# Performance work log

Hardware: AMD Instinct MI355X
Metric: run time of the kernel (lower is better)

Reference implementation:

```python
import jax, jax.numpy as jnp
import numpy as np

B, S, E = 4, 2048, 1024
H, D = 16, 64
SCALE = D ** -0.5


def setup_inputs() -> dict:
    key = jax.random.key(0)
    ks = jax.random.split(key, 6)
    x = jax.random.normal(ks[0], (B, S, E), dtype=jnp.float32)
    # per-head projection weights stacked along head axis: [H, E, D]
    Wq = jax.random.normal(ks[1], (H, E, D), dtype=jnp.float32) * 0.02
    Wk = jax.random.normal(ks[2], (H, E, D), dtype=jnp.float32) * 0.02
    Wv = jax.random.normal(ks[3], (H, E, D), dtype=jnp.float32) * 0.02
    # output projection: concat(H*D) -> E, with bias (nn.Linear default)
    Wo = jax.random.normal(ks[4], (H * D, E), dtype=jnp.float32) * 0.02
    bo = jax.random.normal(ks[5], (E,), dtype=jnp.float32) * 0.02
    return {"x": x, "Wq": Wq, "Wk": Wk, "Wv": Wv, "Wo": Wo, "bo": bo}


def reference(x, Wq, Wk, Wv, Wo, bo):
    # batched QKV projections for all heads at once
    q = jnp.einsum('bse,hed->bhsd', x, Wq)
    k = jnp.einsum('bse,hed->bhsd', x, Wk)
    v = jnp.einsum('bse,hed->bhsd', x, Wv)
    # full (non-causal) attention, scores [b,h,s,s]
    scores = jnp.einsum('bhsd,bhtd->bhst', q, k) * SCALE
    attn = jax.nn.softmax(scores, axis=-1)
    o = jnp.einsum('bhst,bhtd->bhsd', attn, v)
    # concat heads in head order along feature dim -> [b,s,H*D]
    o = o.transpose(0, 2, 1, 3).reshape(x.shape[0], x.shape[1], -1)
    return o @ Wo + bo
```

## Files before the change

### kernel.cpp

```cpp
#include <hip/hip_runtime.h>
#include <hip/hip_fp16.h>
#include <stdint.h>

#define BB 4
#define SS 2048
#define EE 1024
#define HH 16
#define DD 64

typedef _Float16 half8 __attribute__((ext_vector_type(8)));
typedef __fp16 fp16x2 __attribute__((ext_vector_type(2)));
typedef float f32x2 __attribute__((ext_vector_type(2)));
typedef float f32x4 __attribute__((ext_vector_type(4)));
typedef float f32x16 __attribute__((ext_vector_type(16)));
typedef uint32_t u32;
typedef uint32_t u32x2 __attribute__((ext_vector_type(2)));

#define MFMA32(a, b, c) __builtin_amdgcn_mfma_f32_16x16x32_f16((a), (b), (c), 0, 0, 0)
#define MFMA3216(a, b, c) __builtin_amdgcn_mfma_f32_32x32x16_f16((a), (b), (c), 0, 0, 0)

#define GLD_LDS16(g, l)                                                        \
  __builtin_amdgcn_global_load_lds(                                            \
      (const __attribute__((address_space(1))) u32*)(const void*)(g),          \
      (__attribute__((address_space(3))) u32*)(void*)(l), 16, 0, 0)

static __device__ __forceinline__ u32 pkh(float a, float b) {
  union { fp16x2 h; u32 u; } z;
  z.h = __builtin_amdgcn_cvt_pkrtz(a, b);
  return z.u;
}

static __device__ __forceinline__ void plswap(u32& a, u32& b) {
  asm("v_permlane32_swap_b32 %0, %1" : "+v"(a), "+v"(b));
}

__global__ __launch_bounds__(256) void conv_x_k(const float* __restrict__ x,
                                                _Float16* __restrict__ xh) {
  size_t i = ((size_t)blockIdx.x * 256 + threadIdx.x) * 8;
  f32x4 a = *(const f32x4*)(x + i);
  f32x4 b = *(const f32x4*)(x + i + 4);
  half8 o;
  o[0] = (_Float16)a[0]; o[1] = (_Float16)a[1];
  o[2] = (_Float16)a[2]; o[3] = (_Float16)a[3];
  o[4] = (_Float16)b[0]; o[5] = (_Float16)b[1];
  o[6] = (_Float16)b[2]; o[7] = (_Float16)b[3];
  *(half8*)(xh + i) = o;
}

__global__ __launch_bounds__(256) void conv_w_k(const float* __restrict__ Wq,
                                                const float* __restrict__ Wk,
                                                const float* __restrict__ Wv,
                                                _Float16* __restrict__ Wt) {
  __shared__ float T[64][65];
  int bid = blockIdx.x;
  int sel = bid >> 8, rem = bid & 255;
  int h = rem >> 4, e0 = (rem & 15) * 64;
  const float* W = (sel == 0 ? Wq : sel == 1 ? Wk : Wv) + (size_t)h * EE * DD;
  float scale = (sel == 0) ? 0.18033688011112042f : 1.0f;
  int tid = threadIdx.x;
  {
    int e = tid >> 2, d0 = (tid & 3) * 16;
#pragma unroll
    for (int i = 0; i < 4; ++i) {
      f32x4 v = *(const f32x4*)(W + (size_t)(e0 + e) * DD + d0 + i * 4);
      T[e][d0 + i * 4 + 0] = v[0];
      T[e][d0 + i * 4 + 1] = v[1];
      T[e][d0 + i * 4 + 2] = v[2];
      T[e][d0 + i * 4 + 3] = v[3];
    }
  }
  __syncthreads();
  {
    int d = tid >> 2, c0 = (tid & 3) * 16;
    half8 o0, o1;
#pragma unroll
    for (int i = 0; i < 8; ++i) o0[i] = (_Float16)(T[c0 + i][d] * scale);
#pragma unroll
    for (int i = 0; i < 8; ++i) o1[i] = (_Float16)(T[c0 + 8 + i][d] * scale);
    _Float16* dst = Wt + ((size_t)sel * 1024 + h * 64 + d) * EE + e0 + c0;
    *(half8*)dst = o0;
    *(half8*)(dst + 8) = o1;
  }
}

__global__ __launch_bounds__(256) void conv_wo_k(const float* __restrict__ Wo,
                                                 _Float16* __restrict__ Wot) {
  __shared__ float T[64][65];
  int bid = blockIdx.x;
  int k0 = (bid >> 4) * 64, n0 = (bid & 15) * 64;
  int tid = threadIdx.x;
  {
    int k = tid >> 2, c0 = (tid & 3) * 16;
#pragma unroll
    for (int i = 0; i < 4; ++i) {
      f32x4 v = *(const f32x4*)(Wo + (size_t)(k0 + k) * EE + n0 + c0 + i * 4);
      T[k][c0 + i * 4 + 0] = v[0];
      T[k][c0 + i * 4 + 1] = v[1];
      T[k][c0 + i * 4 + 2] = v[2];
      T[k][c0 + i * 4 + 3] = v[3];
    }
  }
  __syncthreads();
  {
    int n = tid >> 2, c0 = (tid & 3) * 16;
    half8 o0, o1;
#pragma unroll
    for (int i = 0; i < 8; ++i) o0[i] = (_Float16)T[c0 + i][n];
#pragma unroll
    for (int i = 0; i < 8; ++i) o1[i] = (_Float16)T[c0 + 8 + i][n];
    _Float16* dst = Wot + (size_t)(n0 + n) * EE + k0 + c0;
    *(half8*)dst = o0;
    *(half8*)(dst + 8) = o1;
  }
}

__global__ __launch_bounds__(256) void vtrans_k(const _Float16* __restrict__ v,
                                                _Float16* __restrict__ vT) {
  __shared__ _Float16 T[64][72];
  int bid = blockIdx.x;
  int bh = bid >> 5, st = bid & 31;
  const _Float16* vp = v + (size_t)bh * SS * DD + (size_t)st * 64 * DD;
  _Float16* op = vT + (size_t)bh * DD * SS + (size_t)st * 64;
  int tid = threadIdx.x;
  {
    int r = tid >> 2, c0 = (tid & 3) * 16;
    half8 a = *(const half8*)(vp + (size_t)r * DD + c0);
    half8 b = *(const half8*)(vp + (size_t)r * DD + c0 + 8);
#pragma unroll
    for (int j = 0; j < 8; ++j) T[c0 + j][r] = a[j];
#pragma unroll
    for (int j = 0; j < 8; ++j) T[c0 + 8 + j][r] = b[j];
  }
  __syncthreads();
  {
    int d = tid >> 2, sc = (tid & 3) * 16;
    half8 o0 = *(const half8*)&T[d][sc];
    half8 o1 = *(const half8*)&T[d][sc + 8];
    *(half8*)(op + (size_t)d * SS + sc) = o0;
    *(half8*)(op + (size_t)d * SS + sc + 8) = o1;
  }
}

__global__ __launch_bounds__(256, 3) void qkv_proj_k(
    const _Float16* __restrict__ xh, const _Float16* __restrict__ Wt,
    _Float16* __restrict__ qkv) {
  __shared__ __align__(16) _Float16 As[128 * 32];
  __shared__ __align__(16) _Float16 Bs[128 * 32];
  int bid0 = blockIdx.x;
  int bid = (bid0 & 7) * 192 + (bid0 >> 3);
  int nblk = bid % 24, mblk = bid / 24;
  int row0 = mblk * 128, n0 = nblk * 128;
  int tid = threadIdx.x, lane = tid & 63, w = tid >> 6;
  int wm = w >> 1, wn = w & 1;
  int l15 = lane & 15, lhi = lane >> 4;

  f32x4 acc[4][4];
#pragma unroll
  for (int i = 0; i < 4; ++i)
#pragma unroll
    for (int j = 0; j < 4; ++j) acc[i][j] = (f32x4){0.f, 0.f, 0.f, 0.f};

  const char* Ab = (const char*)xh + (size_t)row0 * 2048;
  const char* Bb = (const char*)Wt + (size_t)n0 * 2048;
  int ob0 = w * 1024 + lane * 16;

  for (int k0 = 0; k0 < EE; k0 += 32) {
    __syncthreads();
    GLD_LDS16(Ab + (size_t)(ob0 >> 6) * 2048 + k0 * 2 + (ob0 & 63),
              (char*)As + w * 1024);
    GLD_LDS16(Ab + (size_t)((ob0 + 4096) >> 6) * 2048 + k0 * 2 + (ob0 & 63),
              (char*)As + 4096 + w * 1024);
    GLD_LDS16(Bb + (size_t)(ob0 >> 6) * 2048 + k0 * 2 + (ob0 & 63),
              (char*)Bs + w * 1024);
    GLD_LDS16(Bb + (size_t)((ob0 + 4096) >> 6) * 2048 + k0 * 2 + (ob0 & 63),
              (char*)Bs + 4096 + w * 1024);
    __syncthreads();
    half8 a[4], b[4];
#pragma unroll
    for (int mf = 0; mf < 4; ++mf)
      a[mf] = *(const half8*)(As + (wm * 64 + mf * 16 + l15) * 32 + 8 * lhi);
#pragma unroll
    for (int nf = 0; nf < 4; ++nf)
      b[nf] = *(const half8*)(Bs + (wn * 64 + nf * 16 + l15) * 32 + 8 * lhi);
#pragma unroll
    for (int mf = 0; mf < 4; ++mf)
#pragma unroll
      for (int nf = 0; nf < 4; ++nf)
        acc[mf][nf] = MFMA32(a[mf], b[nf], acc[mf][nf]);
  }

  const size_t KOFF = (size_t)BB * HH * SS * DD;
#pragma unroll
  for (int mf = 0; mf < 4; ++mf)
#pragma unroll
    for (int nf = 0; nf < 4; ++nf)
#pragma unroll
      for (int r = 0; r < 4; ++r) {
        int row = row0 + wm * 64 + mf * 16 + 4 * lhi + r;
        int n = n0 + wn * 64 + nf * 16 + l15;
        int sel = n >> 10, hh = (n >> 6) & 15, d = n & 63;
        int b_ = row >> 11, s = row & 2047;
        qkv[(size_t)sel * KOFF + (((size_t)b_ * HH + hh) * SS + s) * DD + d] =
            (_Float16)acc[mf][nf][r];
      }
}

__global__ __launch_bounds__(512, 1) void attn_k(
    const _Float16* __restrict__ qkv, const _Float16* __restrict__ vT,
    _Float16* __restrict__ ob) {
  __shared__ __align__(16) _Float16 Ks[2][64 * 64];
  __shared__ __align__(16) _Float16 Vs[2][64 * 64];

  const int bid0 = blockIdx.x;
  const int bid = (bid0 & 7) * 32 + (bid0 >> 3);
  const int bh = bid >> 2, qb = bid & 3;
  const int b_ = bh >> 4, h = bh & 15;
  const size_t KOFF = (size_t)BB * HH * SS * DD;
  const _Float16* qp = qkv + (size_t)bh * SS * DD;
  const char* kp = (const char*)(qkv + KOFF + (size_t)bh * SS * DD);
  const char* vtp = (const char*)(vT + (size_t)bh * DD * SS);

  const int tid = threadIdx.x, lane = tid & 63, w = tid >> 6;
  const int l31 = lane & 31, u = lane >> 5;
  const int q0 = qb * 512 + w * 64;

  half8 qf[4][2];
#pragma unroll
  for (int ekf = 0; ekf < 4; ++ekf)
#pragma unroll
    for (int nq = 0; nq < 2; ++nq)
      qf[ekf][nq] = *(const half8*)(qp +
          (size_t)(q0 + nq * 32 + l31) * DD + ekf * 16 + u * 8);

  f32x16 oa00 = {}, oa10 = {}, oa01 = {}, oa11 = {};
  f32x2 rs2_0 = {0.f, 0.f}, rs2_1 = {0.f, 0.f};

  const int trow = tid >> 3;
  const int scol = ((tid & 7) * 16) ^ (16 * (trow & 7));
  const int lds0 = tid * 16;
  const int xsw = 16 * (l31 & 7);
  const int NT = SS / 64;

  GLD_LDS16(kp + trow * 128 + scol, (char*)Ks[0] + lds0);
  GLD_LDS16(vtp + (size_t)trow * 4096 + scol, (char*)Vs[0] + lds0);
  __syncthreads();

  for (int it = 0; it < NT; ++it) {
    const int cur = it & 1;
    if (it + 1 < NT) {
      GLD_LDS16(kp + (size_t)(it + 1) * 8192 + trow * 128 + scol,
                (char*)Ks[cur ^ 1] + lds0);
      GLD_LDS16(vtp + (size_t)(it + 1) * 128 + (size_t)trow * 4096 + scol,
                (char*)Vs[cur ^ 1] + lds0);
    }
    const char* kb = (const char*)Ks[cur];
    const char* vb = (const char*)Vs[cur];

#pragma unroll
    for (int nt = 0; nt < 2; ++nt) {
      const char* krow = kb + (size_t)(32 * nt + l31) * 128;
      half8 kA0 = *(const half8*)(krow + ((16 * u) ^ xsw));
      half8 kA1 = *(const half8*)(krow + ((32 + 16 * u) ^ xsw));
      half8 kA2 = *(const half8*)(krow + ((64 + 16 * u) ^ xsw));
      half8 kA3 = *(const half8*)(krow + ((96 + 16 * u) ^ xsw));
      f32x16 s0 = {}, s1 = {};
      __builtin_amdgcn_s_setprio(1);
      s0 = MFMA3216(kA0, qf[0][0], s0);
      s1 = MFMA3216(kA0, qf[0][1], s1);
      s0 = MFMA3216(kA1, qf[1][0], s0);
      s1 = MFMA3216(kA1, qf[1][1], s1);
      s0 = MFMA3216(kA2, qf[2][0], s0);
      s1 = MFMA3216(kA2, qf[2][1], s1);
      s0 = MFMA3216(kA3, qf[3][0], s0);
      s1 = MFMA3216(kA3, qf[3][1], s1);
      __builtin_amdgcn_s_setprio(0);

      u32 w0[8], w1[8];
#pragma unroll
      for (int m = 0; m < 8; ++m) {
        float a0 = __builtin_amdgcn_exp2f(s0[2 * m]);
        float a1 = __builtin_amdgcn_exp2f(s0[2 * m + 1]);
        w0[m] = pkh(a0, a1);
        rs2_0 += (f32x2){a0, a1};
        float c0 = __builtin_amdgcn_exp2f(s1[2 * m]);
        float c1 = __builtin_amdgcn_exp2f(s1[2 * m + 1]);
        w1[m] = pkh(c0, c1);
        rs2_1 += (f32x2){c0, c1};
      }

#pragma unroll
      for (int kfl = 0; kfl < 2; ++kfl) {
        u32 p00 = w0[4 * kfl + 0], p02 = w0[4 * kfl + 2];
        u32 p01 = w0[4 * kfl + 1], p03 = w0[4 * kfl + 3];
        plswap(p00, p02);
        plswap(p01, p03);
        u32 p10 = w1[4 * kfl + 0], p12 = w1[4 * kfl + 2];
        u32 p11 = w1[4 * kfl + 1], p13 = w1[4 * kfl + 3];
        plswap(p10, p12);
        plswap(p11, p13);
        union { u32 q[4]; half8 h; } pb0, pb1;
        pb0.q[0] = p00; pb0.q[1] = p01; pb0.q[2] = p02; pb0.q[3] = p03;
        pb1.q[0] = p10; pb1.q[1] = p11; pb1.q[2] = p12; pb1.q[3] = p13;
        const int kf = 2 * nt + kfl;
        const char* vcol = vb + ((32 * kf + 16 * u) ^ xsw);
        half8 vA0 = *(const half8*)(vcol + (size_t)l31 * 128);
        half8 vA1 = *(const half8*)(vcol + (size_t)(32 + l31) * 128);
        __builtin_amdgcn_s_setprio(1);
        oa00 = MFMA3216(vA0, pb0.h, oa00);
        oa10 = MFMA3216(vA1, pb0.h, oa10);
        oa01 = MFMA3216(vA0, pb1.h, oa01);
        oa11 = MFMA3216(vA1, pb1.h, oa11);
        __builtin_amdgcn_s_setprio(0);
      }
    }
    __syncthreads();
  }

  float rs0 = rs2_0.x + rs2_0.y;
  float rs1 = rs2_1.x + rs2_1.y;
  float inv0 = 1.0f / (rs0 + __shfl_xor(rs0, 32, 64));
  float inv1 = 1.0f / (rs1 + __shfl_xor(rs1, 32, 64));

#define STORE_OA(OA, MD, NQ, INV)                                              \
  {                                                                            \
    _Float16* dst = ob + (size_t)(b_ * SS + q0 + 32 * (NQ) + l31) * 1024 +     \
                    h * 64 + 32 * (MD) + 4 * u;                                \
    _Pragma("unroll")                                                          \
    for (int rr = 0; rr < 4; ++rr) {                                           \
      u32x2 pr;                                                                \
      pr.x = pkh(OA[4 * rr + 0] * (INV), OA[4 * rr + 1] * (INV));              \
      pr.y = pkh(OA[4 * rr + 2] * (INV), OA[4 * rr + 3] * (INV));              \
      *(u32x2*)(dst + 8 * rr) = pr;                                            \
    }                                                                          \
  }
  STORE_OA(oa00, 0, 0, inv0)
  STORE_OA(oa10, 1, 0, inv0)
  STORE_OA(oa01, 0, 1, inv1)
  STORE_OA(oa11, 1, 1, inv1)
#undef STORE_OA
}

__global__ __launch_bounds__(256, 3) void oproj_k(
    const _Float16* __restrict__ ob, const _Float16* __restrict__ Wot,
    const float* __restrict__ bo, float* __restrict__ out) {
  __shared__ __align__(16) _Float16 As[128 * 32];
  __shared__ __align__(16) _Float16 Bs[128 * 32];
  int bid0 = blockIdx.x;
  int bid = (bid0 & 7) * 64 + (bid0 >> 3);
  int nblk = bid & 7, mblk = bid >> 3;
  int row0 = mblk * 128, n0 = nblk * 128;
  int tid = threadIdx.x, lane = tid & 63, w = tid >> 6;
  int wm = w >> 1, wn = w & 1;
  int l15 = lane & 15, lhi = lane >> 4;

  f32x4 acc[4][4];
#pragma unroll
  for (int i = 0; i < 4; ++i)
#pragma unroll
    for (int j = 0; j < 4; ++j) acc[i][j] = (f32x4){0.f, 0.f, 0.f, 0.f};

  const char* Ab = (const char*)ob + (size_t)row0 * 2048;
  const char* Bb = (const char*)Wot + (size_t)n0 * 2048;
  int ob0 = w * 1024 + lane * 16;

  for (int k0 = 0; k0 < EE; k0 += 32) {
    __syncthreads();
    GLD_LDS16(Ab + (size_t)(ob0 >> 6) * 2048 + k0 * 2 + (ob0 & 63),
              (char*)As + w * 1024);
    GLD_LDS16(Ab + (size_t)((ob0 + 4096) >> 6) * 2048 + k0 * 2 + (ob0 & 63),
              (char*)As + 4096 + w * 1024);
    GLD_LDS16(Bb + (size_t)(ob0 >> 6) * 2048 + k0 * 2 + (ob0 & 63),
              (char*)Bs + w * 1024);
    GLD_LDS16(Bb + (size_t)((ob0 + 4096) >> 6) * 2048 + k0 * 2 + (ob0 & 63),
              (char*)Bs + 4096 + w * 1024);
    __syncthreads();
    half8 a[4], b[4];
#pragma unroll
    for (int mf = 0; mf < 4; ++mf)
      a[mf] = *(const half8*)(As + (wm * 64 + mf * 16 + l15) * 32 + 8 * lhi);
#pragma unroll
    for (int nf = 0; nf < 4; ++nf)
      b[nf] = *(const half8*)(Bs + (wn * 64 + nf * 16 + l15) * 32 + 8 * lhi);
#pragma unroll
    for (int mf = 0; mf < 4; ++mf)
#pragma unroll
      for (int nf = 0; nf < 4; ++nf)
        acc[mf][nf] = MFMA32(a[mf], b[nf], acc[mf][nf]);
  }

#pragma unroll
  for (int mf = 0; mf < 4; ++mf)
#pragma unroll
    for (int nf = 0; nf < 4; ++nf) {
      int n = n0 + wn * 64 + nf * 16 + l15;
      float bias = bo[n];
#pragma unroll
      for (int r = 0; r < 4; ++r) {
        int row = row0 + wm * 64 + mf * 16 + 4 * lhi + r;
        out[(size_t)row * EE + n] = acc[mf][nf][r] + bias;
      }
    }
}

extern "C" void kernel_launch(void* const* d_in, const int* in_sizes, int n_in,
                              void* d_out, int out_size, void* d_ws, size_t ws_size,
                              hipStream_t stream) {
  const float* x  = (const float*)d_in[0];
  const float* Wq = (const float*)d_in[1];
  const float* Wk = (const float*)d_in[2];
  const float* Wv = (const float*)d_in[3];
  const float* Wo = (const float*)d_in[4];
  const float* bo = (const float*)d_in[5];
  float* out = (float*)d_out;

  const size_t KOFF = (size_t)BB * HH * SS * DD;
  _Float16* qkv = (_Float16*)d_ws;
  _Float16* obuf = qkv + 3 * KOFF;
  _Float16* xh = (_Float16*)d_out;
  _Float16* Wt = xh + (size_t)BB * SS * EE;
  _Float16* vTbuf = xh;
  _Float16* Wot = qkv;

  conv_x_k<<<dim3(4096), dim3(256), 0, stream>>>(x, xh);
  conv_w_k<<<dim3(768), dim3(256), 0, stream>>>(Wq, Wk, Wv, Wt);
  qkv_proj_k<<<dim3(64 * 24), dim3(256), 0, stream>>>(xh, Wt, qkv);
  vtrans_k<<<dim3(64 * 32), dim3(256), 0, stream>>>(qkv + 2 * KOFF, vTbuf);
  attn_k<<<dim3(256), dim3(512), 0, stream>>>(qkv, vTbuf, obuf);
  conv_wo_k<<<dim3(256), dim3(256), 0, stream>>>(Wo, Wot);
  oproj_k<<<dim3(64 * 8), dim3(256), 0, stream>>>(obuf, Wot, bo, out);
}
```

Baseline: 196.9 us.

## Fuse V transpose into QKV GEMM epilogue, double-buffer GEMMs, reshape attention blocks

The V output of the QKV projection is now transposed through LDS inside the GEMM epilogue and written directly in [b,h,d,s] layout, so the separate vtrans kernel and its extra global round-trip go away. Both GEMMs (QKV and output projection) get double-buffered LDS staging so the next K-slice loads while the current one is multiplied. The attention kernel moves from 512-thread single-block CUs to 256-thread blocks with two per CU, and a grid of 512. It also drops the s_setprio hints. The added LDS for the transpose tile and double buffers may reduce occupancy of the GEMM kernels.

```diff
diff --git a/kernel.cpp b/kernel.cpp
--- a/kernel.cpp
+++ b/kernel.cpp
@@ -114,38 +114,12 @@
   }
 }
 
-__global__ __launch_bounds__(256) void vtrans_k(const _Float16* __restrict__ v,
-                                                _Float16* __restrict__ vT) {
-  __shared__ _Float16 T[64][72];
-  int bid = blockIdx.x;
-  int bh = bid >> 5, st = bid & 31;
-  const _Float16* vp = v + (size_t)bh * SS * DD + (size_t)st * 64 * DD;
-  _Float16* op = vT + (size_t)bh * DD * SS + (size_t)st * 64;
-  int tid = threadIdx.x;
-  {
-    int r = tid >> 2, c0 = (tid & 3) * 16;
-    half8 a = *(const half8*)(vp + (size_t)r * DD + c0);
-    half8 b = *(const half8*)(vp + (size_t)r * DD + c0 + 8);
-#pragma unroll
-    for (int j = 0; j < 8; ++j) T[c0 + j][r] = a[j];
-#pragma unroll
-    for (int j = 0; j < 8; ++j) T[c0 + 8 + j][r] = b[j];
-  }
-  __syncthreads();
-  {
-    int d = tid >> 2, sc = (tid & 3) * 16;
-    half8 o0 = *(const half8*)&T[d][sc];
-    half8 o1 = *(const half8*)&T[d][sc + 8];
-    *(half8*)(op + (size_t)d * SS + sc) = o0;
-    *(half8*)(op + (size_t)d * SS + sc + 8) = o1;
-  }
-}
-
 __global__ __launch_bounds__(256, 3) void qkv_proj_k(
     const _Float16* __restrict__ xh, const _Float16* __restrict__ Wt,
     _Float16* __restrict__ qkv) {
-  __shared__ __align__(16) _Float16 As[128 * 32];
-  __shared__ __align__(16) _Float16 Bs[128 * 32];
+  __shared__ __align__(16) _Float16 As[2][128 * 32];
+  __shared__ __align__(16) _Float16 Bs[2][128 * 32];
+  __shared__ __align__(16) _Float16 Tt[64][136];
   int bid0 = blockIdx.x;
   int bid = (bid0 & 7) * 192 + (bid0 >> 3);
   int nblk = bid % 24, mblk = bid / 24;
@@ -164,65 +138,101 @@
   const char* Bb = (const char*)Wt + (size_t)n0 * 2048;
   int ob0 = w * 1024 + lane * 16;
 
+#define STAGE_AB(K0, BUF)                                                      \
+  {                                                                            \
+    GLD_LDS16(Ab + (size_t)(ob0 >> 6) * 2048 + (K0) * 2 + (ob0 & 63),          \
+              (char*)As[BUF] + w * 1024);                                      \
+    GLD_LDS16(Ab + (size_t)((ob0 + 4096) >> 6) * 2048 + (K0) * 2 + (ob0 & 63), \
+              (char*)As[BUF] + 4096 + w * 1024);                               \
+    GLD_LDS16(Bb + (size_t)(ob0 >> 6) * 2048 + (K0) * 2 + (ob0 & 63),          \
+              (char*)Bs[BUF] + w * 1024);                                      \
+    GLD_LDS16(Bb + (size_t)((ob0 + 4096) >> 6) * 2048 + (K0) * 2 + (ob0 & 63), \
+              (char*)Bs[BUF] + 4096 + w * 1024);                               \
+  }
+
+  STAGE_AB(0, 0);
+  __syncthreads();
+
   for (int k0 = 0; k0 < EE; k0 += 32) {
-    __syncthreads();
-    GLD_LDS16(Ab + (size_t)(ob0 >> 6) * 2048 + k0 * 2 + (ob0 & 63),
-              (char*)As + w * 1024);
-    GLD_LDS16(Ab + (size_t)((ob0 + 4096) >> 6) * 2048 + k0 * 2 + (ob0 & 63),
-              (char*)As + 4096 + w * 1024);
-    GLD_LDS16(Bb + (size_t)(ob0 >> 6) * 2048 + k0 * 2 + (ob0 & 63),
-              (char*)Bs + w * 1024);
-    GLD_LDS16(Bb + (size_t)((ob0 + 4096) >> 6) * 2048 + k0 * 2 + (ob0 & 63),
-              (char*)Bs + 4096 + w * 1024);
-    __syncthreads();
+    int cur = (k0 >> 5) & 1;
+    if (k0 + 32 < EE) STAGE_AB(k0 + 32, cur ^ 1);
     half8 a[4], b[4];
 #pragma unroll
     for (int mf = 0; mf < 4; ++mf)
-      a[mf] = *(const half8*)(As + (wm * 64 + mf * 16 + l15) * 32 + 8 * lhi);
+      a[mf] = *(const half8*)(As[cur] + (wm * 64 + mf * 16 + l15) * 32 + 8 * lhi);
 #pragma unroll
     for (int nf = 0; nf < 4; ++nf)
-      b[nf] = *(const half8*)(Bs + (wn * 64 + nf * 16 + l15) * 32 + 8 * lhi);
+      b[nf] = *(const half8*)(Bs[cur] + (wn * 64 + nf * 16 + l15) * 32 + 8 * lhi);
 #pragma unroll
     for (int mf = 0; mf < 4; ++mf)
 #pragma unroll
       for (int nf = 0; nf < 4; ++nf)
         acc[mf][nf] = MFMA32(a[mf], b[nf], acc[mf][nf]);
-  }
+    __syncthreads();
+  }
+#undef STAGE_AB
 
   const size_t KOFF = (size_t)BB * HH * SS * DD;
-#pragma unroll
-  for (int mf = 0; mf < 4; ++mf)
-#pragma unroll
-    for (int nf = 0; nf < 4; ++nf)
-#pragma unroll
-      for (int r = 0; r < 4; ++r) {
-        int row = row0 + wm * 64 + mf * 16 + 4 * lhi + r;
-        int n = n0 + wn * 64 + nf * 16 + l15;
-        int sel = n >> 10, hh = (n >> 6) & 15, d = n & 63;
-        int b_ = row >> 11, s = row & 2047;
-        qkv[(size_t)sel * KOFF + (((size_t)b_ * HH + hh) * SS + s) * DD + d] =
-            (_Float16)acc[mf][nf][r];
+  if (nblk < 16) {
+#pragma unroll
+    for (int mf = 0; mf < 4; ++mf)
+#pragma unroll
+      for (int nf = 0; nf < 4; ++nf)
+#pragma unroll
+        for (int r = 0; r < 4; ++r) {
+          int row = row0 + wm * 64 + mf * 16 + 4 * lhi + r;
+          int n = n0 + wn * 64 + nf * 16 + l15;
+          int sel = n >> 10, hh = (n >> 6) & 15, d = n & 63;
+          int b_ = row >> 11, s = row & 2047;
+          qkv[(size_t)sel * KOFF + (((size_t)b_ * HH + hh) * SS + s) * DD + d] =
+              (_Float16)acc[mf][nf][r];
+        }
+  } else {
+    int b_ = row0 >> 11, sbase = row0 & 2047;
+    _Float16* vout = qkv + 2 * KOFF;
+#pragma unroll
+    for (int half = 0; half < 2; ++half) {
+      if (half) __syncthreads();
+      if (wn == half) {
+#pragma unroll
+        for (int mf = 0; mf < 4; ++mf)
+#pragma unroll
+          for (int nf = 0; nf < 4; ++nf) {
+            union { _Float16 h[4]; u32x2 v; } t4;
+#pragma unroll
+            for (int r = 0; r < 4; ++r) t4.h[r] = (_Float16)acc[mf][nf][r];
+            *(u32x2*)&Tt[nf * 16 + l15][wm * 64 + mf * 16 + 4 * lhi] = t4.v;
+          }
       }
-}
-
-__global__ __launch_bounds__(512, 1) void attn_k(
-    const _Float16* __restrict__ qkv, const _Float16* __restrict__ vT,
-    _Float16* __restrict__ ob) {
+      __syncthreads();
+      int d = tid >> 2, c0 = (tid & 3) * 32;
+      int head = ((n0 >> 6) + half) & 15;
+      _Float16* dst =
+          vout + ((size_t)((b_ * 16 + head) * 64 + d)) * SS + sbase + c0;
+#pragma unroll
+      for (int j = 0; j < 4; ++j)
+        *(half8*)(dst + 8 * j) = *(const half8*)&Tt[d][c0 + 8 * j];
+    }
+  }
+}
+
+__global__ __launch_bounds__(256, 2) void attn_k(
+    const _Float16* __restrict__ qkv, _Float16* __restrict__ ob) {
   __shared__ __align__(16) _Float16 Ks[2][64 * 64];
   __shared__ __align__(16) _Float16 Vs[2][64 * 64];
 
   const int bid0 = blockIdx.x;
-  const int bid = (bid0 & 7) * 32 + (bid0 >> 3);
-  const int bh = bid >> 2, qb = bid & 3;
+  const int bid = (bid0 & 7) * 64 + (bid0 >> 3);
+  const int bh = bid >> 3, qb = bid & 7;
   const int b_ = bh >> 4, h = bh & 15;
   const size_t KOFF = (size_t)BB * HH * SS * DD;
   const _Float16* qp = qkv + (size_t)bh * SS * DD;
   const char* kp = (const char*)(qkv + KOFF + (size_t)bh * SS * DD);
-  const char* vtp = (const char*)(vT + (size_t)bh * DD * SS);
+  const char* vtp = (const char*)(qkv + 2 * KOFF + (size_t)bh * DD * SS);
 
   const int tid = threadIdx.x, lane = tid & 63, w = tid >> 6;
   const int l31 = lane & 31, u = lane >> 5;
-  const int q0 = qb * 512 + w * 64;
+  const int q0 = qb * 256 + w * 64;
 
   half8 qf[4][2];
 #pragma unroll
@@ -241,18 +251,23 @@
   const int xsw = 16 * (l31 & 7);
   const int NT = SS / 64;
 
-  GLD_LDS16(kp + trow * 128 + scol, (char*)Ks[0] + lds0);
-  GLD_LDS16(vtp + (size_t)trow * 4096 + scol, (char*)Vs[0] + lds0);
+#define STAGE_KV(IT, BUF)                                                      \
+  {                                                                            \
+    const char* sk_ = kp + (size_t)(IT) * 8192;                                \
+    const char* sv_ = vtp + (size_t)(IT) * 128;                                \
+    GLD_LDS16(sk_ + trow * 128 + scol, (char*)Ks[BUF] + lds0);                 \
+    GLD_LDS16(sk_ + (trow + 32) * 128 + scol, (char*)Ks[BUF] + 4096 + lds0);   \
+    GLD_LDS16(sv_ + (size_t)trow * 4096 + scol, (char*)Vs[BUF] + lds0);        \
+    GLD_LDS16(sv_ + (size_t)(trow + 32) * 4096 + scol,                         \
+              (char*)Vs[BUF] + 4096 + lds0);                                   \
+  }
+
+  STAGE_KV(0, 0);
   __syncthreads();
 
   for (int it = 0; it < NT; ++it) {
     const int cur = it & 1;
-    if (it + 1 < NT) {
-      GLD_LDS16(kp + (size_t)(it + 1) * 8192 + trow * 128 + scol,
-                (char*)Ks[cur ^ 1] + lds0);
-      GLD_LDS16(vtp + (size_t)(it + 1) * 128 + (size_t)trow * 4096 + scol,
-                (char*)Vs[cur ^ 1] + lds0);
-    }
+    if (it + 1 < NT) STAGE_KV(it + 1, cur ^ 1);
     const char* kb = (const char*)Ks[cur];
     const char* vb = (const char*)Vs[cur];
 
@@ -264,7 +279,6 @@
       half8 kA2 = *(const half8*)(krow + ((64 + 16 * u) ^ xsw));
       half8 kA3 = *(const half8*)(krow + ((96 + 16 * u) ^ xsw));
       f32x16 s0 = {}, s1 = {};
-      __builtin_amdgcn_s_setprio(1);
       s0 = MFMA3216(kA0, qf[0][0], s0);
       s1 = MFMA3216(kA0, qf[0][1], s1);
       s0 = MFMA3216(kA1, qf[1][0], s0);
@@ -273,7 +287,6 @@
       s1 = MFMA3216(kA2, qf[2][1], s1);
       s0 = MFMA3216(kA3, qf[3][0], s0);
       s1 = MFMA3216(kA3, qf[3][1], s1);
-      __builtin_amdgcn_s_setprio(0);
 
       u32 w0[8], w1[8];
 #pragma unroll
@@ -305,16 +318,15 @@
         const char* vcol = vb + ((32 * kf + 16 * u) ^ xsw);
         half8 vA0 = *(const half8*)(vcol + (size_t)l31 * 128);
         half8 vA1 = *(const half8*)(vcol + (size_t)(32 + l31) * 128);
-        __builtin_amdgcn_s_setprio(1);
         oa00 = MFMA3216(vA0, pb0.h, oa00);
         oa10 = MFMA3216(vA1, pb0.h, oa10);
         oa01 = MFMA3216(vA0, pb1.h, oa01);
         oa11 = MFMA3216(vA1, pb1.h, oa11);
-        __builtin_amdgcn_s_setprio(0);
       }
     }
     __syncthreads();
   }
+#undef STAGE_KV
 
   float rs0 = rs2_0.x + rs2_0.y;
   float rs1 = rs2_1.x + rs2_1.y;
@@ -343,8 +355,8 @@
 __global__ __launch_bounds__(256, 3) void oproj_k(
     const _Float16* __restrict__ ob, const _Float16* __restrict__ Wot,
     const float* __restrict__ bo, float* __restrict__ out) {
-  __shared__ __align__(16) _Float16 As[128 * 32];
-  __shared__ __align__(16) _Float16 Bs[128 * 32];
+  __shared__ __align__(16) _Float16 As[2][128 * 32];
+  __shared__ __align__(16) _Float16 Bs[2][128 * 32];
   int bid0 = blockIdx.x;
   int bid = (bid0 & 7) * 64 + (bid0 >> 3);
   int nblk = bid & 7, mblk = bid >> 3;
@@ -363,30 +375,39 @@
   const char* Bb = (const char*)Wot + (size_t)n0 * 2048;
   int ob0 = w * 1024 + lane * 16;
 
+#define STAGE_AB(K0, BUF)                                                      \
+  {                                                                            \
+    GLD_LDS16(Ab + (size_t)(ob0 >> 6) * 2048 + (K0) * 2 + (ob0 & 63),          \
+              (char*)As[BUF] + w * 1024);                                      \
+    GLD_LDS16(Ab + (size_t)((ob0 + 4096) >> 6) * 2048 + (K0) * 2 + (ob0 & 63), \
+              (char*)As[BUF] + 4096 + w * 1024);                               \
+    GLD_LDS16(Bb + (size_t)(ob0 >> 6) * 2048 + (K0) * 2 + (ob0 & 63),          \
+              (char*)Bs[BUF] + w * 1024);                                      \
+    GLD_LDS16(Bb + (size_t)((ob0 + 4096) >> 6) * 2048 + (K0) * 2 + (ob0 & 63), \
+              (char*)Bs[BUF] + 4096 + w * 1024);                               \
+  }
+
+  STAGE_AB(0, 0);
+  __syncthreads();
+
   for (int k0 = 0; k0 < EE; k0 += 32) {
-    __syncthreads();
-    GLD_LDS16(Ab + (size_t)(ob0 >> 6) * 2048 + k0 * 2 + (ob0 & 63),
-              (char*)As + w * 1024);
-    GLD_LDS16(Ab + (size_t)((ob0 + 4096) >> 6) * 2048 + k0 * 2 + (ob0 & 63),
-              (char*)As + 4096 + w * 1024);
-    GLD_LDS16(Bb + (size_t)(ob0 >> 6) * 2048 + k0 * 2 + (ob0 & 63),
-              (char*)Bs + w * 1024);
-    GLD_LDS16(Bb + (size_t)((ob0 + 4096) >> 6) * 2048 + k0 * 2 + (ob0 & 63),
-              (char*)Bs + 4096 + w * 1024);
-    __syncthreads();
+    int cur = (k0 >> 5) & 1;
+    if (k0 + 32 < EE) STAGE_AB(k0 + 32, cur ^ 1);
     half8 a[4], b[4];
 #pragma unroll
     for (int mf = 0; mf < 4; ++mf)
-      a[mf] = *(const half8*)(As + (wm * 64 + mf * 16 + l15) * 32 + 8 * lhi);
+      a[mf] = *(const half8*)(As[cur] + (wm * 64 + mf * 16 + l15) * 32 + 8 * lhi);
 #pragma unroll
     for (int nf = 0; nf < 4; ++nf)
-      b[nf] = *(const half8*)(Bs + (wn * 64 + nf * 16 + l15) * 32 + 8 * lhi);
+      b[nf] = *(const half8*)(Bs[cur] + (wn * 64 + nf * 16 + l15) * 32 + 8 * lhi);
 #pragma unroll
     for (int mf = 0; mf < 4; ++mf)
 #pragma unroll
       for (int nf = 0; nf < 4; ++nf)
         acc[mf][nf] = MFMA32(a[mf], b[nf], acc[mf][nf]);
-  }
+    __syncthreads();
+  }
+#undef STAGE_AB
 
 #pragma unroll
   for (int mf = 0; mf < 4; ++mf)
@@ -418,14 +439,12 @@
   _Float16* obuf = qkv + 3 * KOFF;
   _Float16* xh = (_Float16*)d_out;
   _Float16* Wt = xh + (size_t)BB * SS * EE;
-  _Float16* vTbuf = xh;
   _Float16* Wot = qkv;
 
   conv_x_k<<<dim3(4096), dim3(256), 0, stream>>>(x, xh);
   conv_w_k<<<dim3(768), dim3(256), 0, stream>>>(Wq, Wk, Wv, Wt);
   qkv_proj_k<<<dim3(64 * 24), dim3(256), 0, stream>>>(xh, Wt, qkv);
-  vtrans_k<<<dim3(64 * 32), dim3(256), 0, stream>>>(qkv + 2 * KOFF, vTbuf);
-  attn_k<<<dim3(256), dim3(512), 0, stream>>>(qkv, vTbuf, obuf);
+  attn_k<<<dim3(512), dim3(256), 0, stream>>>(qkv, obuf);
   conv_wo_k<<<dim3(256), dim3(256), 0, stream>>>(Wo, Wot);
   oproj_k<<<dim3(64 * 8), dim3(256), 0, stream>>>(obuf, Wot, bo, out);
 }
```

Result: faster. 187.3 us (median of 2 runs) (-4.8%).
